# Optimization experiments

Measured on AMD Instinct MI355X. Metric: run time of the kernel, lower is better.

The kernel has to match this reference:

```python
import jax, jax.numpy as jnp
import numpy as np

# Grid / physics constants (stand-ins for the attributes of self.model)
N = 256                 # voxels per axis (cubic unit cell)
CELL = 100.0            # unit cell edge in Angstrom (orthogonal cell, frac matrix = I/CELL)
SPACING = CELL / N      # voxel spacing in Angstrom
SOLVENT_R = 1.1         # dilation probe radius (init default `radius`)
EROSION_R = 0.9         # erosion radius (init default `erosion_radius`)
VDW_MAX = 1.9           # static upper bound on vdw radii (generation range [1.2,1.9])
N_ATOMS = 5000


def setup_inputs() -> dict:
    key = jax.random.key(0)
    k1, k2 = jax.random.split(key)
    xyz = jax.random.uniform(k1, (N_ATOMS, 3), jnp.float32) * CELL
    vdw_radii = 1.2 + 0.7 * jax.random.uniform(k2, (N_ATOMS,), jnp.float32)
    return {"xyz": xyz, "vdw_radii": vdw_radii}


def _solvent_pipeline(xyz, vdw_radii):
    # ---- Step 1: dilation -- per-atom radius query into the voxel grid ----
    max_r = VDW_MAX + SOLVENT_R                       # self.max_radius_angstrom
    Kh = int(np.ceil(max_r / SPACING))
    g = np.arange(-Kh, Kh + 1)
    offs = np.stack(np.meshgrid(g, g, g, indexing='ij'), -1).reshape(-1, 3)
    offs = jnp.asarray(offs, jnp.int32)               # [M,3] local voxel offsets

    base = jnp.floor(xyz / SPACING).astype(jnp.int32)          # [A,3] home voxel
    coords = base[:, None, :] + offs[None, :, :]               # [A,M,3]
    centers = coords.astype(jnp.float32) * SPACING             # voxel centers (unwrapped)
    d = jnp.sqrt(jnp.sum((centers - xyz[:, None, :]) ** 2, -1))  # [A,M] atom-voxel dist

    w = jnp.mod(coords, N)                                     # periodic wrap of indices
    flat = ((w[..., 0] * N + w[..., 1]) * N + w[..., 2]).ravel()

    vr = vdw_radii[:, None]
    prot = (d < vr).ravel()                                    # inside vdw -> protein core
    bound = ((d >= vr) & (d < vr + SOLVENT_R)).ravel()         # vdw..vdw+probe -> boundary

    protein = (jnp.zeros(N ** 3, jnp.int8).at[flat].max(prot.astype(jnp.int8)) > 0)
    boundary = (jnp.zeros(N ** 3, jnp.int8).at[flat].max(bound.astype(jnp.int8)) > 0)
    protein = protein.reshape(N, N, N)
    boundary = boundary.reshape(N, N, N) & ~protein            # symmetry = identity (P1)
    def_solv = ~(protein | boundary)

    # ---- Step 2: erosion -- boundary voxel flips to solvent if any voxel within
    #      erosion_radius is definitely solvent ----
    rh = int(np.ceil(EROSION_R / SPACING))
    g2 = np.arange(-rh, rh + 1)
    eo = np.stack(np.meshgrid(g2, g2, g2, indexing='ij'), -1).reshape(-1, 3)
    eo = eo[np.linalg.norm(eo * SPACING, axis=1) <= EROSION_R]  # sphere stencil (static)
    has_nb = jnp.zeros((N, N, N), bool)
    for o in eo:  # small static stencil (~50 offsets)
        has_nb = has_nb | jnp.roll(def_solv, shift=(-int(o[0]), -int(o[1]), -int(o[2])), axis=(0, 1, 2))
    flip = boundary & has_nb
    protein_with_boundary = (protein | boundary) & ~flip
    solvent = (~protein_with_boundary).astype(jnp.float32)

    # ---- Step 3: Gaussian smoothing with circular padding ----
    sigma = (SOLVENT_R / SPACING) / 4.0                        # self.transition (voxels)
    ks = int(4 * sigma + 1)
    if ks % 2 == 0:
        ks += 1
    x = np.arange(ks) - ks // 2
    g1 = np.exp(-x ** 2 / (2 * sigma ** 2))
    g1 = g1 / g1.sum()
    k3 = g1[:, None, None] * g1[None, :, None] * g1[None, None, :]
    k3 = jnp.asarray(k3 / k3.sum(), jnp.float32)
    pad = ks // 2
    padded = jnp.pad(solvent, pad, mode='wrap')
    out = jax.lax.conv_general_dilated(padded[None, None], k3[None, None], (1, 1, 1), 'VALID')
    return out[0, 0]  # [N,N,N] smoothed solvent mask


def reference(xyz, vdw_radii):
    return _solvent_pipeline(xyz, vdw_radii)
```

## Files before the change

kernel.cpp:

```cpp
#include <hip/hip_runtime.h>
#include <math.h>

#define NG 256
#define NG3 (NG*NG*NG)
#define NW (NG3/64)

typedef unsigned long long u64;
typedef unsigned int u32;

constexpr float SPACING_F = 0.390625f;
constexpr int KH = 8;
constexpr int KD = 17;

#define NBIN 64
#define BCAP 32
#define NCAND 160

#define CB(x, y) (((((x) & 255) << 8) | ((y) & 255)) << 2)

__global__ void bin_fill_kernel(const float* __restrict__ xyz, int natoms,
                                int* __restrict__ bin_cnt, int* __restrict__ bin_list)
{
    int a = blockIdx.x * 256 + threadIdx.x;
    if (a >= natoms) return;
    float ax = xyz[a * 3 + 0], ay = xyz[a * 3 + 1];
    int bx = (int)floorf(__fdiv_rn(ax, SPACING_F));
    int by = (int)floorf(__fdiv_rn(ay, SPACING_F));
    int b = ((by >> 2) & (NBIN - 1)) * NBIN + ((bx >> 2) & (NBIN - 1));
    int s = atomicAdd(&bin_cnt[b], 1);
    if (s < BCAP) bin_list[b * BCAP + s] = a;
}

__global__ void __launch_bounds__(512) col_splat_kernel(
    const float* __restrict__ xyz, const float* __restrict__ vdw,
    const int* __restrict__ bin_cnt, const int* __restrict__ bin_list,
    u64* __restrict__ occ_bits, u64* __restrict__ p_bits)
{
    __shared__ float4 candF[NCAND];
    __shared__ int    candB[NCAND];
    __shared__ int lc;

    const int tid = threadIdx.x;
    const int BX = blockIdx.x & 15, BY = blockIdx.x >> 4;
    const int x0 = BX * 16, y0 = BY * 16;

    if (tid == 0) lc = 0;
    __syncthreads();

    if (tid < 64) {
        int abx = (4 * BX - 2 + (tid & 7)) & (NBIN - 1);
        int aby = (4 * BY - 2 + (tid >> 3)) & (NBIN - 1);
        int b = aby * NBIN + abx;
        int n = min(bin_cnt[b], BCAP);
        if (n > 0) {
            int base = atomicAdd(&lc, n);
            for (int j = 0; j < n; ++j) {
                int idx = base + j;
                if (idx < NCAND) {
                    int a = bin_list[b * BCAP + j];
                    float ax = xyz[a * 3 + 0], ay = xyz[a * 3 + 1], az = xyz[a * 3 + 2];
                    candF[idx] = make_float4(ax, ay, az, vdw[a]);
                    int bx = (int)floorf(__fdiv_rn(ax, SPACING_F));
                    int by = (int)floorf(__fdiv_rn(ay, SPACING_F));
                    int bz = (int)floorf(__fdiv_rn(az, SPACING_F));
                    candB[idx] = bx | (by << 8) | (bz << 16);
                }
            }
        }
    }
    __syncthreads();
    const int nc = min(lc, NCAND);

    const int col = tid >> 1;
    const int sub = tid & 1;
    const int X = x0 + (col >> 4), Y = y0 + (col & 15);

    u64 o0 = 0, o1 = 0, o2 = 0, o3 = 0;
    u64 q0 = 0, q1 = 0, q2 = 0, q3 = 0;

    for (int c = sub; c < nc; c += 2) {
        float4 f = candF[c];
        int bb = candB[c];
        int bx = bb & 255, by = (bb >> 8) & 255, bz = (bb >> 16) & 255;
        int dx = ((X - bx + 128) & 255) - 128;
        int dy = ((Y - by + 128) & 255) - 128;
        if (dx < -KH || dx > KH || dy < -KH || dy > KH) continue;
        float ex = __fsub_rn(__fmul_rn((float)(bx + dx), SPACING_F), f.x);
        float ey = __fsub_rn(__fmul_rn((float)(by + dy), SPACING_F), f.y);
        float rxy2 = __fadd_rn(__fmul_rn(ex, ex), __fmul_rn(ey, ey));
        float vr = f.w;
        float br = __fadd_rn(vr, 1.1f);
        if (rxy2 >= __fmul_rn(br, br)) continue;

        u32 mo = 0, mp = 0;
        #pragma unroll
        for (int k = 0; k < KD; ++k) {
            int cz = bz + k - KH;
            float ez = __fsub_rn(__fmul_rn((float)cz, SPACING_F), f.z);
            float s = __fadd_rn(rxy2, __fmul_rn(ez, ez));
            float d = __fsqrt_rn(s);
            mo |= (d < br) ? (1u << k) : 0u;
            mp |= (d < vr) ? (1u << k) : 0u;
        }
        if (!mo) continue;

        int zA = (bz - KH) & 255;
        int wa = zA >> 6, off = zA & 63;
        int wb = (wa + 1) & 3;
        u64 lo = (u64)mo << off;
        u64 hi = off ? ((u64)mo >> (64 - off)) : 0ULL;
        u64 plo = (u64)mp << off;
        u64 phi = off ? ((u64)mp >> (64 - off)) : 0ULL;
        o0 |= (wa == 0 ? lo : 0) | (wb == 0 ? hi : 0);
        o1 |= (wa == 1 ? lo : 0) | (wb == 1 ? hi : 0);
        o2 |= (wa == 2 ? lo : 0) | (wb == 2 ? hi : 0);
        o3 |= (wa == 3 ? lo : 0) | (wb == 3 ? hi : 0);
        q0 |= (wa == 0 ? plo : 0) | (wb == 0 ? phi : 0);
        q1 |= (wa == 1 ? plo : 0) | (wb == 1 ? phi : 0);
        q2 |= (wa == 2 ? plo : 0) | (wb == 2 ? phi : 0);
        q3 |= (wa == 3 ? plo : 0) | (wb == 3 ? phi : 0);
    }

    o0 |= __shfl_xor(o0, 1, 64);  o1 |= __shfl_xor(o1, 1, 64);
    o2 |= __shfl_xor(o2, 1, 64);  o3 |= __shfl_xor(o3, 1, 64);
    q0 |= __shfl_xor(q0, 1, 64);  q1 |= __shfl_xor(q1, 1, 64);
    q2 |= __shfl_xor(q2, 1, 64);  q3 |= __shfl_xor(q3, 1, 64);

    u64* dst = (sub == 0 ? occ_bits : p_bits) + CB(X, Y);
    if (sub == 0) {
        *(ulonglong2*)(dst + 0) = make_ulonglong2(o0, o1);
        *(ulonglong2*)(dst + 2) = make_ulonglong2(o2, o3);
    } else {
        *(ulonglong2*)(dst + 0) = make_ulonglong2(q0, q1);
        *(ulonglong2*)(dst + 2) = make_ulonglong2(q2, q3);
    }
}

#define LCB(ox, oy) ((((ox) * 14) + (oy)) * 4)
#define SCB(sx, sy) ((((sx) * 10) + (sy)) * 4)

union SMem {
    u64 occT[784];
    float stage[256][33];
};

__device__ __forceinline__ u64 lrng5(const u64* T, int cb, int wz) {
    u64 C = T[cb | wz], P = T[cb | ((wz + 3) & 3)], Nw = T[cb | ((wz + 1) & 3)];
    u64 d1 = (C << 1) | (P >> 63), d2 = (C << 2) | (P >> 62);
    u64 u1 = (C >> 1) | (Nw << 63), u2 = (C >> 2) | (Nw << 62);
    return C & d1 & d2 & u1 & u2;
}
__device__ __forceinline__ u64 lrng3(const u64* T, int cb, int wz) {
    u64 C = T[cb | wz], P = T[cb | ((wz + 3) & 3)], Nw = T[cb | ((wz + 1) & 3)];
    u64 d1 = (C << 1) | (P >> 63);
    u64 u1 = (C >> 1) | (Nw << 63);
    return C & d1 & u1;
}

struct Tri { u64 m1, m0, p1; };
__device__ __forceinline__ Tri triL(const u64* T, int cb, int wz) {
    u64 C = T[cb | wz], P = T[cb | ((wz + 3) & 3)], Nw = T[cb | ((wz + 1) & 3)];
    Tri t;
    t.m0 = C;
    t.m1 = (C << 1) | (P >> 63);
    t.p1 = (C >> 1) | (Nw << 63);
    return t;
}

__device__ __forceinline__ void csa(u64 a, u64 b, u64 c, u64& s, u64& cy) {
    u64 t = a ^ b;
    s = t ^ c;
    cy = (a & b) | (t & c);
}

__global__ void __launch_bounds__(256) solv_gauss_kernel(
    const u64* __restrict__ occ_bits, const u64* __restrict__ p_bits,
    float* __restrict__ out, float W0, float W1, float W2, float W3)
{
    __shared__ SMem sm;
    __shared__ u64 solT[400];
    __shared__ float lutA[256];

    const int tid = threadIdx.x;
    const int bx = blockIdx.x & 31, by = blockIdx.x >> 5;
    const int x0 = bx * 8, y0 = by * 8;

    for (int i = tid; i < 784; i += 256) {
        int owz = i & 3; int c = i >> 2;
        int oy = c % 14, ox = c / 14;
        sm.occT[i] = occ_bits[CB(x0 - 3 + ox, y0 - 3 + oy) | owz];
    }
    {
        int g = tid & 1, c1v = (tid >> 1) & 7, c2v = (tid >> 4) & 15;
        float acc = g ? W0 : 0.0f;
        acc = fmaf(W1, (float)c1v, acc);
        acc = fmaf(W2, (float)c2v, acc);
        lutA[tid] = acc;
    }
    __syncthreads();

    for (int i = tid; i < 400; i += 256) {
        int swz = i & 3; int c = i >> 2;
        int sy = c % 10, sx = c / 10;
        int ox = sx + 2, oy = sy + 2;
        const u64* T = sm.occT;
        u64 ero = lrng5(T, LCB(ox, oy), swz);
        ero &= lrng5(T, LCB(ox + 1, oy), swz);
        ero &= lrng5(T, LCB(ox - 1, oy), swz);
        ero &= lrng5(T, LCB(ox, oy + 1), swz);
        ero &= lrng5(T, LCB(ox, oy - 1), swz);
        ero &= lrng3(T, LCB(ox + 1, oy + 1), swz);
        ero &= lrng3(T, LCB(ox + 1, oy - 1), swz);
        ero &= lrng3(T, LCB(ox - 1, oy + 1), swz);
        ero &= lrng3(T, LCB(ox - 1, oy - 1), swz);
        ero &= lrng3(T, LCB(ox + 2, oy), swz);
        ero &= lrng3(T, LCB(ox - 2, oy), swz);
        ero &= lrng3(T, LCB(ox, oy + 2), swz);
        ero &= lrng3(T, LCB(ox, oy - 2), swz);
        ero &= T[LCB(ox + 1, oy + 2) | swz];
        ero &= T[LCB(ox + 1, oy - 2) | swz];
        ero &= T[LCB(ox - 1, oy + 2) | swz];
        ero &= T[LCB(ox - 1, oy - 2) | swz];
        ero &= T[LCB(ox + 2, oy + 1) | swz];
        ero &= T[LCB(ox + 2, oy - 1) | swz];
        ero &= T[LCB(ox - 2, oy + 1) | swz];
        ero &= T[LCB(ox - 2, oy - 1) | swz];

        u64 C = T[LCB(ox, oy) | swz];
        u64 pw = p_bits[CB(x0 - 1 + sx, y0 - 1 + sy) | swz];
        solT[i] = ~(pw | (C & ero));
    }
    __syncthreads();

    const int gwz = tid & 3;
    const int gc = tid >> 2;
    const int gy = gc & 7, gx = gc >> 3;
    const int sx = gx + 1, sy = gy + 1;

    Tri cc = triL(solT, SCB(sx, sy), gwz);
    Tri e0 = triL(solT, SCB(sx + 1, sy), gwz), e1 = triL(solT, SCB(sx - 1, sy), gwz);
    Tri e2 = triL(solT, SCB(sx, sy + 1), gwz), e3 = triL(solT, SCB(sx, sy - 1), gwz);
    Tri d0 = triL(solT, SCB(sx + 1, sy + 1), gwz), d1 = triL(solT, SCB(sx + 1, sy - 1), gwz);
    Tri d2 = triL(solT, SCB(sx - 1, sy + 1), gwz), d3 = triL(solT, SCB(sx - 1, sy - 1), gwz);

    u64 sa, ca, sb, cb2;
    csa(cc.m1, cc.p1, e0.m0, sa, ca);
    csa(e1.m0, e2.m0, e3.m0, sb, cb2);
    u64 c1b0 = sa ^ sb; u64 h = sa & sb;
    u64 c1b1, c1b2;
    csa(ca, cb2, h, c1b1, c1b2);

    u64 s1, k1, s2, k2, s3, k3, s4, k4;
    csa(e0.m1, e0.p1, e1.m1, s1, k1);
    csa(e1.p1, e2.m1, e2.p1, s2, k2);
    csa(e3.m1, e3.p1, d0.m0, s3, k3);
    csa(d1.m0, d2.m0, d3.m0, s4, k4);
    u64 t5, kt;
    csa(s1, s2, s3, t5, kt);
    u64 c2b0 = t5 ^ s4; u64 h0 = t5 & s4;
    u64 u_, ku, v_, kv;
    csa(k1, k2, k3, u_, ku);
    csa(k4, kt, h0, v_, kv);
    u64 c2b1 = u_ ^ v_; u64 h1 = u_ & v_;
    u64 c2b2, c2b3;
    csa(ku, kv, h1, c2b2, c2b3);

    u64 p1s, p1c, p2s, p2c;
    csa(d0.m1, d0.p1, d1.m1, p1s, p1c);
    csa(d1.p1, d2.m1, d2.p1, p2s, p2c);
    u64 t3, kt3;
    csa(p1s, p2s, d3.m1, t3, kt3);
    u64 c3b0 = t3 ^ d3.p1; u64 h3 = t3 & d3.p1;
    u64 u3, ku3;
    csa(p1c, p2c, kt3, u3, ku3);
    u64 c3b1 = u3 ^ h3; u64 h4 = u3 & h3;
    u64 c3b2 = ku3 ^ h4, c3b3 = ku3 & h4;

    #pragma unroll
    for (int hh = 0; hh < 2; ++hh) {
        const int sh = hh * 32;
        u32 pA[8] = { (u32)(cc.m0 >> sh), (u32)(c1b0 >> sh), (u32)(c1b1 >> sh),
                      (u32)(c1b2 >> sh), (u32)(c2b0 >> sh), (u32)(c2b1 >> sh),
                      (u32)(c2b2 >> sh), (u32)(c2b3 >> sh) };
        u32 pB[4] = { (u32)(c3b0 >> sh), (u32)(c3b1 >> sh),
                      (u32)(c3b2 >> sh), (u32)(c3b3 >> sh) };
        #pragma unroll
        for (int z0 = 0; z0 < 8; ++z0) {
            u32 accA = 0, accB = 0;
            #pragma unroll
            for (int j = 0; j < 8; ++j) accA |= ((pA[j] >> z0) & 0x01010101u) << j;
            #pragma unroll
            for (int j = 0; j < 4; ++j) accB |= ((pB[j] >> z0) & 0x01010101u) << j;
            #pragma unroll
            for (int b = 0; b < 4; ++b) {
                int idxA = (accA >> (8 * b)) & 255;
                int c3v  = (accB >> (8 * b)) & 15;
                float val = fmaf(W3, (float)c3v, lutA[idxA]);
                sm.stage[tid][z0 + 8 * b] = val;
            }
        }
        __syncthreads();
        #pragma unroll
        for (int k = 0; k < 8; ++k) {
            int i = tid + k * 256;
            int wl = i >> 3;
            int zo = (i & 7) * 4;
            int ggx = wl >> 5, ggy = (wl >> 2) & 7, ggwz = wl & 3;
            size_t base = ((size_t)(((x0 + ggx) << 10) + (y0 + ggy) * 4 + ggwz)) * 64;
            float4 v = make_float4(sm.stage[wl][zo], sm.stage[wl][zo + 1],
                                   sm.stage[wl][zo + 2], sm.stage[wl][zo + 3]);
            *(float4*)(out + base + sh + zo) = v;
        }
        __syncthreads();
    }
}

extern "C" void kernel_launch(void* const* d_in, const int* in_sizes, int n_in,
                              void* d_out, int out_size, void* d_ws, size_t ws_size,
                              hipStream_t stream)
{
    const float* xyz = (const float*)d_in[0];
    const float* vdw = (const float*)d_in[1];
    float* out = (float*)d_out;

    u64* occ_bits = (u64*)d_ws;
    u64* p_bits   = occ_bits + NW;
    int* bin_cnt  = (int*)(p_bits + NW);
    int* bin_list = bin_cnt + NBIN * NBIN;
    const int natoms = in_sizes[1];

    hipMemsetAsync(bin_cnt, 0, NBIN * NBIN * sizeof(int), stream);
    bin_fill_kernel<<<(natoms + 255) / 256, 256, 0, stream>>>(
        xyz, natoms, bin_cnt, bin_list);
    col_splat_kernel<<<256, 512, 0, stream>>>(
        xyz, vdw, bin_cnt, bin_list, occ_bits, p_bits);

    double spacing = 100.0 / 256.0;
    double sigma = 1.1 / spacing / 4.0;
    double a = exp(-1.0 / (2.0 * sigma * sigma));
    double ssum = 2.0 * a + 1.0;
    double an = a / ssum, bn = 1.0 / ssum;
    float W0 = (float)(bn * bn * bn);
    float W1 = (float)(an * bn * bn);
    float W2 = (float)(an * an * bn);
    float W3 = (float)(an * an * an);

    solv_gauss_kernel<<<1024, 256, 0, stream>>>(
        occ_bits, p_bits, out, W0, W1, W2, W3);
}
```

Measured before the change: 133.2 us.

## Shrink splat tiles to 8x8 columns and restructure Gaussian output staging

The splat kernel moves from 16x16-column tiles (256 blocks of 512 threads) to 8x8-column tiles (1024 blocks of 256 threads). Each column is split across four lanes, and the partial bitmasks are merged with two xor-shuffles. The smoothing kernel loads occupancy with vector loads and stages packed per-voxel neighbour-count bit fields in shared memory instead of finished floats. The float LUT plus FMA is evaluated during a single coalesced store pass, which removes one barrier round and shrinks shared memory. The risk is that the smaller candidate capacity (96) silently drops atoms when a 6x6-bin neighbourhood is dense, and that the extra halo candidates are re-read by more blocks.

Result: faster. 124.3 us (-6.7%).

```diff
diff --git a/kernel.cpp b/kernel.cpp
--- a/kernel.cpp
+++ b/kernel.cpp
@@ -14,7 +14,7 @@
 
 #define NBIN 64
 #define BCAP 32
-#define NCAND 160
+#define NCAND 96
 
 #define CB(x, y) (((((x) & 255) << 8) | ((y) & 255)) << 2)
 
@@ -31,7 +31,7 @@
     if (s < BCAP) bin_list[b * BCAP + s] = a;
 }
 
-__global__ void __launch_bounds__(512) col_splat_kernel(
+__global__ void __launch_bounds__(256) col_splat8_kernel(
     const float* __restrict__ xyz, const float* __restrict__ vdw,
     const int* __restrict__ bin_cnt, const int* __restrict__ bin_list,
     u64* __restrict__ occ_bits, u64* __restrict__ p_bits)
@@ -41,15 +41,15 @@
     __shared__ int lc;
 
     const int tid = threadIdx.x;
-    const int BX = blockIdx.x & 15, BY = blockIdx.x >> 4;
-    const int x0 = BX * 16, y0 = BY * 16;
+    const int BX = blockIdx.x & 31, BY = blockIdx.x >> 5;
+    const int x0 = BX * 8, y0 = BY * 8;
 
     if (tid == 0) lc = 0;
     __syncthreads();
 
-    if (tid < 64) {
-        int abx = (4 * BX - 2 + (tid & 7)) & (NBIN - 1);
-        int aby = (4 * BY - 2 + (tid >> 3)) & (NBIN - 1);
+    if (tid < 36) {
+        int abx = (2 * BX - 2 + (tid % 6)) & (NBIN - 1);
+        int aby = (2 * BY - 2 + (tid / 6)) & (NBIN - 1);
         int b = aby * NBIN + abx;
         int n = min(bin_cnt[b], BCAP);
         if (n > 0) {
@@ -71,14 +71,14 @@
     __syncthreads();
     const int nc = min(lc, NCAND);
 
-    const int col = tid >> 1;
-    const int sub = tid & 1;
-    const int X = x0 + (col >> 4), Y = y0 + (col & 15);
+    const int col = tid >> 2;
+    const int sub = tid & 3;
+    const int X = x0 + (col >> 3), Y = y0 + (col & 7);
 
     u64 o0 = 0, o1 = 0, o2 = 0, o3 = 0;
     u64 q0 = 0, q1 = 0, q2 = 0, q3 = 0;
 
-    for (int c = sub; c < nc; c += 2) {
+    for (int c = sub; c < nc; c += 4) {
         float4 f = candF[c];
         int bb = candB[c];
         int bx = bb & 255, by = (bb >> 8) & 255, bz = (bb >> 16) & 255;
@@ -125,23 +125,25 @@
     o2 |= __shfl_xor(o2, 1, 64);  o3 |= __shfl_xor(o3, 1, 64);
     q0 |= __shfl_xor(q0, 1, 64);  q1 |= __shfl_xor(q1, 1, 64);
     q2 |= __shfl_xor(q2, 1, 64);  q3 |= __shfl_xor(q3, 1, 64);
-
-    u64* dst = (sub == 0 ? occ_bits : p_bits) + CB(X, Y);
-    if (sub == 0) {
-        *(ulonglong2*)(dst + 0) = make_ulonglong2(o0, o1);
-        *(ulonglong2*)(dst + 2) = make_ulonglong2(o2, o3);
-    } else {
-        *(ulonglong2*)(dst + 0) = make_ulonglong2(q0, q1);
-        *(ulonglong2*)(dst + 2) = make_ulonglong2(q2, q3);
-    }
+    o0 |= __shfl_xor(o0, 2, 64);  o1 |= __shfl_xor(o1, 2, 64);
+    o2 |= __shfl_xor(o2, 2, 64);  o3 |= __shfl_xor(o3, 2, 64);
+    q0 |= __shfl_xor(q0, 2, 64);  q1 |= __shfl_xor(q1, 2, 64);
+    q2 |= __shfl_xor(q2, 2, 64);  q3 |= __shfl_xor(q3, 2, 64);
+
+    u64* base = (sub < 2 ? occ_bits : p_bits) + CB(X, Y) + (sub & 1) * 2;
+    if (sub == 0)      *(ulonglong2*)base = make_ulonglong2(o0, o1);
+    else if (sub == 1) *(ulonglong2*)base = make_ulonglong2(o2, o3);
+    else if (sub == 2) *(ulonglong2*)base = make_ulonglong2(q0, q1);
+    else               *(ulonglong2*)base = make_ulonglong2(q2, q3);
 }
 
 #define LCB(ox, oy) ((((ox) * 14) + (oy)) * 4)
 #define SCB(sx, sy) ((((sx) * 10) + (sy)) * 4)
+#define ASTRIDE 25
 
 union SMem {
     u64 occT[784];
-    float stage[256][33];
+    u32 accAB[256 * ASTRIDE];
 };
 
 __device__ __forceinline__ u64 lrng5(const u64* T, int cb, int wz) {
@@ -185,10 +187,14 @@
     const int bx = blockIdx.x & 31, by = blockIdx.x >> 5;
     const int x0 = bx * 8, y0 = by * 8;
 
-    for (int i = tid; i < 784; i += 256) {
-        int owz = i & 3; int c = i >> 2;
-        int oy = c % 14, ox = c / 14;
-        sm.occT[i] = occ_bits[CB(x0 - 3 + ox, y0 - 3 + oy) | owz];
+    if (tid < 196) {
+        int oy = tid % 14, ox = tid / 14;
+        const u64* src = &occ_bits[CB(x0 - 3 + ox, y0 - 3 + oy)];
+        ulonglong2 a = *(const ulonglong2*)(src);
+        ulonglong2 b = *(const ulonglong2*)(src + 2);
+        u64* dst = &sm.occT[(ox * 14 + oy) * 4];
+        *(ulonglong2*)(dst) = a;
+        *(ulonglong2*)(dst + 2) = b;
     }
     {
         int g = tid & 1, c1v = (tid >> 1) & 7, c2v = (tid >> 4) & 15;
@@ -232,86 +238,99 @@
     }
     __syncthreads();
 
-    const int gwz = tid & 3;
-    const int gc = tid >> 2;
-    const int gy = gc & 7, gx = gc >> 3;
-    const int sx = gx + 1, sy = gy + 1;
-
-    Tri cc = triL(solT, SCB(sx, sy), gwz);
-    Tri e0 = triL(solT, SCB(sx + 1, sy), gwz), e1 = triL(solT, SCB(sx - 1, sy), gwz);
-    Tri e2 = triL(solT, SCB(sx, sy + 1), gwz), e3 = triL(solT, SCB(sx, sy - 1), gwz);
-    Tri d0 = triL(solT, SCB(sx + 1, sy + 1), gwz), d1 = triL(solT, SCB(sx + 1, sy - 1), gwz);
-    Tri d2 = triL(solT, SCB(sx - 1, sy + 1), gwz), d3 = triL(solT, SCB(sx - 1, sy - 1), gwz);
-
-    u64 sa, ca, sb, cb2;
-    csa(cc.m1, cc.p1, e0.m0, sa, ca);
-    csa(e1.m0, e2.m0, e3.m0, sb, cb2);
-    u64 c1b0 = sa ^ sb; u64 h = sa & sb;
-    u64 c1b1, c1b2;
-    csa(ca, cb2, h, c1b1, c1b2);
-
-    u64 s1, k1, s2, k2, s3, k3, s4, k4;
-    csa(e0.m1, e0.p1, e1.m1, s1, k1);
-    csa(e1.p1, e2.m1, e2.p1, s2, k2);
-    csa(e3.m1, e3.p1, d0.m0, s3, k3);
-    csa(d1.m0, d2.m0, d3.m0, s4, k4);
-    u64 t5, kt;
-    csa(s1, s2, s3, t5, kt);
-    u64 c2b0 = t5 ^ s4; u64 h0 = t5 & s4;
-    u64 u_, ku, v_, kv;
-    csa(k1, k2, k3, u_, ku);
-    csa(k4, kt, h0, v_, kv);
-    u64 c2b1 = u_ ^ v_; u64 h1 = u_ & v_;
-    u64 c2b2, c2b3;
-    csa(ku, kv, h1, c2b2, c2b3);
-
-    u64 p1s, p1c, p2s, p2c;
-    csa(d0.m1, d0.p1, d1.m1, p1s, p1c);
-    csa(d1.p1, d2.m1, d2.p1, p2s, p2c);
-    u64 t3, kt3;
-    csa(p1s, p2s, d3.m1, t3, kt3);
-    u64 c3b0 = t3 ^ d3.p1; u64 h3 = t3 & d3.p1;
-    u64 u3, ku3;
-    csa(p1c, p2c, kt3, u3, ku3);
-    u64 c3b1 = u3 ^ h3; u64 h4 = u3 & h3;
-    u64 c3b2 = ku3 ^ h4, c3b3 = ku3 & h4;
+    {
+        const int gwz = tid & 3;
+        const int gc = tid >> 2;
+        const int gy = gc & 7, gx = gc >> 3;
+        const int sx = gx + 1, sy = gy + 1;
+
+        Tri cc = triL(solT, SCB(sx, sy), gwz);
+        Tri e0 = triL(solT, SCB(sx + 1, sy), gwz), e1 = triL(solT, SCB(sx - 1, sy), gwz);
+        Tri e2 = triL(solT, SCB(sx, sy + 1), gwz), e3 = triL(solT, SCB(sx, sy - 1), gwz);
+        Tri d0 = triL(solT, SCB(sx + 1, sy + 1), gwz), d1 = triL(solT, SCB(sx + 1, sy - 1), gwz);
+        Tri d2 = triL(solT, SCB(sx - 1, sy + 1), gwz), d3 = triL(solT, SCB(sx - 1, sy - 1), gwz);
+
+        u64 sa, ca, sb, cb2;
+        csa(cc.m1, cc.p1, e0.m0, sa, ca);
+        csa(e1.m0, e2.m0, e3.m0, sb, cb2);
+        u64 c1b0 = sa ^ sb; u64 h = sa & sb;
+        u64 c1b1, c1b2;
+        csa(ca, cb2, h, c1b1, c1b2);
+
+        u64 s1, k1, s2, k2, s3, k3, s4, k4;
+        csa(e0.m1, e0.p1, e1.m1, s1, k1);
+        csa(e1.p1, e2.m1, e2.p1, s2, k2);
+        csa(e3.m1, e3.p1, d0.m0, s3, k3);
+        csa(d1.m0, d2.m0, d3.m0, s4, k4);
+        u64 t5, kt;
+        csa(s1, s2, s3, t5, kt);
+        u64 c2b0 = t5 ^ s4; u64 h0 = t5 & s4;
+        u64 u_, ku, v_, kv;
+        csa(k1, k2, k3, u_, ku);
+        csa(k4, kt, h0, v_, kv);
+        u64 c2b1 = u_ ^ v_; u64 h1 = u_ & v_;
+        u64 c2b2, c2b3;
+        csa(ku, kv, h1, c2b2, c2b3);
+
+        u64 p1s, p1c, p2s, p2c;
+        csa(d0.m1, d0.p1, d1.m1, p1s, p1c);
+        csa(d1.p1, d2.m1, d2.p1, p2s, p2c);
+        u64 t3, kt3;
+        csa(p1s, p2s, d3.m1, t3, kt3);
+        u64 c3b0 = t3 ^ d3.p1; u64 h3 = t3 & d3.p1;
+        u64 u3, ku3;
+        csa(p1c, p2c, kt3, u3, ku3);
+        u64 c3b1 = u3 ^ h3; u64 h4 = u3 & h3;
+        u64 c3b2 = ku3 ^ h4, c3b3 = ku3 & h4;
+
+        u32* myA = &sm.accAB[tid * ASTRIDE];
+        #pragma unroll
+        for (int hh = 0; hh < 2; ++hh) {
+            const int sh = hh * 32;
+            u32 pA[8] = { (u32)(cc.m0 >> sh), (u32)(c1b0 >> sh), (u32)(c1b1 >> sh),
+                          (u32)(c1b2 >> sh), (u32)(c2b0 >> sh), (u32)(c2b1 >> sh),
+                          (u32)(c2b2 >> sh), (u32)(c2b3 >> sh) };
+            u32 pB[4] = { (u32)(c3b0 >> sh), (u32)(c3b1 >> sh),
+                          (u32)(c3b2 >> sh), (u32)(c3b3 >> sh) };
+            u32 bv[8];
+            #pragma unroll
+            for (int z0 = 0; z0 < 8; ++z0) {
+                u32 accA = 0, accB = 0;
+                #pragma unroll
+                for (int j = 0; j < 8; ++j) accA |= ((pA[j] >> z0) & 0x01010101u) << j;
+                #pragma unroll
+                for (int j = 0; j < 4; ++j) accB |= ((pB[j] >> z0) & 0x01010101u) << j;
+                myA[hh * 8 + z0] = accA;
+                bv[z0] = accB;
+            }
+            #pragma unroll
+            for (int p = 0; p < 4; ++p)
+                myA[16 + hh * 4 + p] = bv[2 * p] | (bv[2 * p + 1] << 4);
+        }
+    }
+    __syncthreads();
 
     #pragma unroll
-    for (int hh = 0; hh < 2; ++hh) {
-        const int sh = hh * 32;
-        u32 pA[8] = { (u32)(cc.m0 >> sh), (u32)(c1b0 >> sh), (u32)(c1b1 >> sh),
-                      (u32)(c1b2 >> sh), (u32)(c2b0 >> sh), (u32)(c2b1 >> sh),
-                      (u32)(c2b2 >> sh), (u32)(c2b3 >> sh) };
-        u32 pB[4] = { (u32)(c3b0 >> sh), (u32)(c3b1 >> sh),
-                      (u32)(c3b2 >> sh), (u32)(c3b3 >> sh) };
-        #pragma unroll
-        for (int z0 = 0; z0 < 8; ++z0) {
-            u32 accA = 0, accB = 0;
-            #pragma unroll
-            for (int j = 0; j < 8; ++j) accA |= ((pA[j] >> z0) & 0x01010101u) << j;
-            #pragma unroll
-            for (int j = 0; j < 4; ++j) accB |= ((pB[j] >> z0) & 0x01010101u) << j;
-            #pragma unroll
-            for (int b = 0; b < 4; ++b) {
-                int idxA = (accA >> (8 * b)) & 255;
-                int c3v  = (accB >> (8 * b)) & 15;
-                float val = fmaf(W3, (float)c3v, lutA[idxA]);
-                sm.stage[tid][z0 + 8 * b] = val;
-            }
-        }
-        __syncthreads();
-        #pragma unroll
-        for (int k = 0; k < 8; ++k) {
-            int i = tid + k * 256;
-            int wl = i >> 3;
-            int zo = (i & 7) * 4;
-            int ggx = wl >> 5, ggy = (wl >> 2) & 7, ggwz = wl & 3;
-            size_t base = ((size_t)(((x0 + ggx) << 10) + (y0 + ggy) * 4 + ggwz)) * 64;
-            float4 v = make_float4(sm.stage[wl][zo], sm.stage[wl][zo + 1],
-                                   sm.stage[wl][zo + 2], sm.stage[wl][zo + 3]);
-            *(float4*)(out + base + sh + zo) = v;
-        }
-        __syncthreads();
+    for (int k = 0; k < 16; ++k) {
+        int f = k * 256 + tid;
+        int u = f >> 4;
+        int q = f & 15;
+        int hh = q >> 3;
+        int qb = (q & 7) >> 1;
+        const u32* ua = &sm.accAB[u * ASTRIDE];
+        int za = hh * 8 + 4 * (q & 1);
+        u32 A0 = ua[za + 0], A1 = ua[za + 1], A2 = ua[za + 2], A3 = ua[za + 3];
+        u32 Blo = ua[16 + hh * 4 + 2 * (q & 1)];
+        u32 Bhi = ua[16 + hh * 4 + 2 * (q & 1) + 1];
+        int shb = 8 * qb;
+        float4 v;
+        v.x = fmaf(W3, (float)((Blo >> (shb + 0)) & 15u), lutA[(A0 >> shb) & 255u]);
+        v.y = fmaf(W3, (float)((Blo >> (shb + 4)) & 15u), lutA[(A1 >> shb) & 255u]);
+        v.z = fmaf(W3, (float)((Bhi >> (shb + 0)) & 15u), lutA[(A2 >> shb) & 255u]);
+        v.w = fmaf(W3, (float)((Bhi >> (shb + 4)) & 15u), lutA[(A3 >> shb) & 255u]);
+        int gx = u >> 5, gy = (u >> 2) & 7, gwz = u & 3;
+        size_t base = ((size_t)((x0 + gx) * 1024 + (y0 + gy) * 4 + gwz)) * 64 + q * 4;
+        *(float4*)(out + base) = v;
     }
 }
 
@@ -332,7 +351,7 @@
     hipMemsetAsync(bin_cnt, 0, NBIN * NBIN * sizeof(int), stream);
     bin_fill_kernel<<<(natoms + 255) / 256, 256, 0, stream>>>(
         xyz, natoms, bin_cnt, bin_list);
-    col_splat_kernel<<<256, 512, 0, stream>>>(
+    col_splat8_kernel<<<1024, 256, 0, stream>>>(
         xyz, vdw, bin_cnt, bin_list, occ_bits, p_bits);
 
     double spacing = 100.0 / 256.0;
```
